# Performance work log

Hardware: AMD Instinct MI355X
Metric: run time of the kernel (lower is better)

The kernel has to match this reference:

```python
import jax, jax.numpy as jnp
import numpy as np

N_LAYERS = 32
HIDDEN = 1024
INTER = 2816
BATCH = 256
INIT_SCALE = 0.02


def setup_inputs() -> dict:
    key = jax.random.key(0)
    k_h, k_g, k_u, k_d = jax.random.split(key, 4)
    down_std = INIT_SCALE / np.sqrt(2 * N_LAYERS)
    h = jax.random.normal(k_h, (BATCH, N_LAYERS, HIDDEN), dtype=jnp.float32)
    # torch Linear weight layout: (out_features, in_features); stack over experts
    Wg = jax.random.normal(k_g, (N_LAYERS, INTER, HIDDEN), dtype=jnp.float32) * INIT_SCALE
    Wu = jax.random.normal(k_u, (N_LAYERS, INTER, HIDDEN), dtype=jnp.float32) * INIT_SCALE
    Wd = jax.random.normal(k_d, (N_LAYERS, HIDDEN, INTER), dtype=jnp.float32) * down_std
    return {"h": h, "Wg": Wg, "Wu": Wu, "Wd": Wd}


def reference(h, Wg, Wu, Wd):
    # h: (B, N, D); Wg/Wu: (N, I, D); Wd: (N, D, I)
    gate = jnp.einsum("bnd,nid->bni", h, Wg)
    up = jnp.einsum("bnd,nid->bni", h, Wu)
    act = jax.nn.silu(gate) * up            # (B, N, I)
    out = jnp.einsum("bni,ndi->bnd", act, Wd)  # (B, N, D)
    return out
```

## Files before the change

### kernel.cpp

```cpp
#include <hip/hip_runtime.h>
#include <hip/hip_bf16.h>

#define BATCH   256
#define NLAYERS 32
#define HID     1024
#define INTER   2816

typedef __attribute__((ext_vector_type(8))) short bf16x8;
typedef __attribute__((ext_vector_type(4))) float f32x4;
typedef __attribute__((ext_vector_type(4))) int   i32x4;

__device__ __forceinline__ ushort f2bf(float f) {
  __hip_bfloat16 b = __float2bfloat16(f);
  return *reinterpret_cast<ushort*>(&b);
}

__device__ __forceinline__ bf16x8 cvt8(f32x4 a, f32x4 b) {
  bf16x8 o;
  o[0] = (short)f2bf(a[0]); o[1] = (short)f2bf(a[1]);
  o[2] = (short)f2bf(a[2]); o[3] = (short)f2bf(a[3]);
  o[4] = (short)f2bf(b[0]); o[5] = (short)f2bf(b[1]);
  o[6] = (short)f2bf(b[2]); o[7] = (short)f2bf(b[3]);
  return o;
}

__global__ __launch_bounds__(256) void k_pack(
    const float* __restrict__ h, ushort* __restrict__ Xp2) {
  const int pr    = blockIdx.x * 4 + (threadIdx.x >> 6);
  const int b     = pr >> 5;
  const int layer = pr & 31;
  const int lane  = threadIdx.x & 63;
  const float* src = h + (size_t)b * (NLAYERS * HID) + (size_t)layer * HID;
  ushort* dstL = Xp2 + (size_t)layer * (32 * 8192);
#pragma unroll
  for (int c = 0; c < 2; ++c) {
    int gi = lane + c * 64;
    int t  = gi >> 2, kg = gi & 3;
    f32x4 v0 = *(const f32x4*)(src + t * 32 + kg * 8);
    f32x4 v1 = *(const f32x4*)(src + t * 32 + kg * 8 + 4);
    int f = kg ^ ((b >> 1) & 3);
    *(bf16x8*)(dstL + (size_t)t * 8192 + b * 32 + f * 8) = cvt8(v0, v1);
  }
}

__global__ __launch_bounds__(512, 4) void k_gateup(
    const ushort* __restrict__ Xp2, const float* __restrict__ Wg,
    const float* __restrict__ Wu, ushort* __restrict__ act) {
  const int bid   = blockIdx.x;
  const int layer = bid / (INTER / 64);
  const int it    = bid % (INTER / 64);
  const int i0    = it * 64;
  const int tid   = threadIdx.x;
  const int lane  = tid & 63;
  const int wave  = tid >> 6;
  const int wm    = wave >> 1;
  const int wn    = wave & 1;
  const int r16   = lane & 15;
  const int g4    = lane >> 4;

  __shared__ ushort Al[2][256 * 32];
  __shared__ ushort Bl[2][128 * 32];

  f32x4 acc[4][2][2] = {};

  const int brow  = tid >> 2;
  const int bslot = tid & 3;
  const int bdst  = brow * 32 + ((bslot ^ ((brow >> 1) & 3)) << 3);
  const float* bsrc = (brow < 64 ? Wg + (size_t)(i0 + brow) * HID
                                 : Wu + (size_t)(i0 + brow - 64) * HID)
                      + (size_t)layer * INTER * HID + bslot * 8;

  const ushort* agbase = Xp2 + (size_t)layer * (32 * 8192);

#pragma unroll
  for (int c = 0; c < 2; ++c)
    __builtin_amdgcn_global_load_lds(
        (const void*)(agbase + (wave * 128 + c * 64 + lane) * 8),
        (void*)&Al[0][(wave * 128 + c * 64) * 8], 16, 0, 0);
  {
    f32x4 rb0 = *(const f32x4*)bsrc;
    f32x4 rb1 = *(const f32x4*)(bsrc + 4);
    *(bf16x8*)&Bl[0][bdst] = cvt8(rb0, rb1);
  }
  __syncthreads();

  const int NK = HID / 32;
  int cur = 0;
  for (int t = 0; t < NK; ++t) {
    const int nxt = cur ^ 1;
    f32x4 rb[2];
    if (t + 1 < NK) {
#pragma unroll
      for (int c = 0; c < 2; ++c)
        __builtin_amdgcn_global_load_lds(
            (const void*)(agbase + (size_t)(t + 1) * 8192 +
                          (wave * 128 + c * 64 + lane) * 8),
            (void*)&Al[nxt][(wave * 128 + c * 64) * 8], 16, 0, 0);
      rb[0] = *(const f32x4*)(bsrc + (t + 1) * 32);
      rb[1] = *(const f32x4*)(bsrc + (t + 1) * 32 + 4);
    }

    bf16x8 af[4];
#pragma unroll
    for (int m = 0; m < 4; ++m) {
      int row = wm * 64 + m * 16 + r16;
      af[m] = *(bf16x8*)&Al[cur][row * 32 + ((g4 ^ ((row >> 1) & 3)) << 3)];
    }
#pragma unroll
    for (int n = 0; n < 2; ++n) {
      int rg_ = wn * 32 + n * 16 + r16;
      int ru_ = 64 + rg_;
      bf16x8 bg = *(bf16x8*)&Bl[cur][rg_ * 32 + ((g4 ^ ((rg_ >> 1) & 3)) << 3)];
      bf16x8 bu = *(bf16x8*)&Bl[cur][ru_ * 32 + ((g4 ^ ((ru_ >> 1) & 3)) << 3)];
#pragma unroll
      for (int m = 0; m < 4; ++m) {
        acc[m][n][0] = __builtin_amdgcn_mfma_f32_16x16x32_bf16(af[m], bg, acc[m][n][0], 0, 0, 0);
        acc[m][n][1] = __builtin_amdgcn_mfma_f32_16x16x32_bf16(af[m], bu, acc[m][n][1], 0, 0, 0);
      }
    }

    if (t + 1 < NK)
      *(bf16x8*)&Bl[nxt][bdst] = cvt8(rb[0], rb[1]);
    __syncthreads();
    cur = nxt;
  }

  const int r4 = (lane >> 4) * 4;
#pragma unroll
  for (int m = 0; m < 4; ++m)
#pragma unroll
    for (int n = 0; n < 2; ++n)
#pragma unroll
      for (int r = 0; r < 4; ++r) {
        float g = acc[m][n][0][r];
        float u = acc[m][n][1][r];
        float a = (g / (1.f + __expf(-g))) * u;
        int b = wm * 64 + m * 16 + r4 + r;
        int i = i0 + wn * 32 + n * 16 + r16;
        act[((size_t)layer * BATCH + b) * INTER + i] = f2bf(a);
      }
}

#define BK 64

__global__ __launch_bounds__(512) void k_down(
    const ushort* __restrict__ act, const float* __restrict__ Wd,
    float* __restrict__ out) {
  const int bid   = blockIdx.x;
  const int layer = bid / (HID / 64);
  const int dtile = bid % (HID / 64);
  const int d0    = dtile * 64;
  const int tid   = threadIdx.x;
  const int lane  = tid & 63;
  const int wave  = tid >> 6;
  const int wm    = wave >> 1;
  const int wn    = wave & 1;

  __shared__ ushort lds[BATCH * BK + 64 * BK];
  ushort* Al = lds;
  ushort* Wl = lds + BATCH * BK;

  f32x4 acc[4][2] = {};

  int aldst[4];
  const ushort* asrc[4];
#pragma unroll
  for (int r = 0; r < 4; ++r) {
    int g = tid + 512 * r;
    int arow = g >> 3, akc = g & 7;
    aldst[r] = arow * BK + ((akc ^ (arow & 7)) << 3);
    asrc[r] = act + ((size_t)layer * BATCH + arow) * INTER + akc * 8;
  }
  const int wrow = tid >> 3, wkc = tid & 7;
  const int wldst = wrow * BK + ((wkc ^ (wrow & 7)) << 3);
  const float* wsrc = Wd + (size_t)layer * HID * INTER + (size_t)(d0 + wrow) * INTER + wkc * 8;

  i32x4 ra[4];
  f32x4 rw[2];

#pragma unroll
  for (int r = 0; r < 4; ++r) ra[r] = *(const i32x4*)asrc[r];
  rw[0] = *(const f32x4*)wsrc; rw[1] = *(const f32x4*)(wsrc + 4);

  const int NK = INTER / BK;
  for (int k = 0; k < NK; ++k) {
    __syncthreads();
#pragma unroll
    for (int r = 0; r < 4; ++r) *(i32x4*)&Al[aldst[r]] = ra[r];
    *(bf16x8*)&Wl[wldst] = cvt8(rw[0], rw[1]);
    __syncthreads();

    if (k + 1 < NK) {
      int off = (k + 1) * BK;
#pragma unroll
      for (int r = 0; r < 4; ++r) ra[r] = *(const i32x4*)(asrc[r] + off);
      rw[0] = *(const f32x4*)(wsrc + off); rw[1] = *(const f32x4*)(wsrc + off + 4);
    }

#pragma unroll
    for (int ks = 0; ks < 2; ++ks) {
      const int kg = ks * 4 + (lane >> 4);
      bf16x8 af[4];
#pragma unroll
      for (int m = 0; m < 4; ++m) {
        int row = wm * 64 + m * 16 + (lane & 15);
        af[m] = *(bf16x8*)&Al[row * BK + ((kg ^ (row & 7)) << 3)];
      }
#pragma unroll
      for (int n = 0; n < 2; ++n) {
        int row = wn * 32 + n * 16 + (lane & 15);
        bf16x8 bw = *(bf16x8*)&Wl[row * BK + ((kg ^ (row & 7)) << 3)];
#pragma unroll
        for (int m = 0; m < 4; ++m)
          acc[m][n] = __builtin_amdgcn_mfma_f32_16x16x32_bf16(af[m], bw, acc[m][n], 0, 0, 0);
      }
    }
  }

  const int c16 = lane & 15;
  const int r4  = (lane >> 4) * 4;
#pragma unroll
  for (int m = 0; m < 4; ++m)
#pragma unroll
    for (int n = 0; n < 2; ++n)
#pragma unroll
      for (int r = 0; r < 4; ++r) {
        int b = wm * 64 + m * 16 + r4 + r;
        int d = d0 + wn * 32 + n * 16 + c16;
        out[(size_t)b * (NLAYERS * HID) + (size_t)layer * HID + d] = acc[m][n][r];
      }
}

extern "C" void kernel_launch(void* const* d_in, const int* in_sizes, int n_in,
                              void* d_out, int out_size, void* d_ws, size_t ws_size,
                              hipStream_t stream) {
  const float* h  = (const float*)d_in[0];
  const float* Wg = (const float*)d_in[1];
  const float* Wu = (const float*)d_in[2];
  const float* Wd = (const float*)d_in[3];
  float* out  = (float*)d_out;
  ushort* act = (ushort*)d_ws;
  ushort* Xp2 = (ushort*)d_ws + (size_t)NLAYERS * BATCH * INTER;

  hipLaunchKernelGGL(k_pack, dim3(BATCH * NLAYERS / 4), dim3(256), 0, stream,
                     h, Xp2);
  hipLaunchKernelGGL(k_gateup, dim3(NLAYERS * (INTER / 64)), dim3(512), 0, stream,
                     Xp2, Wg, Wu, act);
  hipLaunchKernelGGL(k_down, dim3(NLAYERS * (HID / 64)), dim3(512), 0, stream,
                     act, Wd, out);
}
```

Baseline: 324.8 us.

## Stream fp32 gate/up weights to LDS asynchronously with triple buffering and smaller tiles

The gate/up kernel now loads fp32 weight tiles directly into LDS with global_load_lds into a three-stage ring buffer. Conversion to bf16 happens after the LDS read instead of before the LDS write, and explicit vmcnt waits with raw barriers replace __syncthreads. The intermediate tile is halved to 32 columns, which doubles the block count, and block IDs are swizzled so that grouped blocks share a layer. The goal is to hide weight-load latency and remove register staging, at the cost of re-reading the activation tile from LDS for each smaller N-tile and doing fewer MFMAs per barrier.

New measurement: 355.8 us. 9.5% more time.

```diff
diff --git a/kernel.cpp b/kernel.cpp
--- a/kernel.cpp
+++ b/kernel.cpp
@@ -47,9 +47,10 @@
     const ushort* __restrict__ Xp2, const float* __restrict__ Wg,
     const float* __restrict__ Wu, ushort* __restrict__ act) {
   const int bid   = blockIdx.x;
-  const int layer = bid / (INTER / 64);
-  const int it    = bid % (INTER / 64);
-  const int i0    = it * 64;
+  const int swz   = (bid & 7) * 352 + (bid >> 3);
+  const int layer = swz / (INTER / 32);
+  const int it    = swz % (INTER / 32);
+  const int i0    = it * 32;
   const int tid   = threadIdx.x;
   const int lane  = tid & 63;
   const int wave  = tid >> 6;
@@ -59,86 +60,86 @@
   const int g4    = lane >> 4;
 
   __shared__ ushort Al[2][256 * 32];
-  __shared__ ushort Bl[2][128 * 32];
-
-  f32x4 acc[4][2][2] = {};
-
-  const int brow  = tid >> 2;
-  const int bslot = tid & 3;
-  const int bdst  = brow * 32 + ((bslot ^ ((brow >> 1) & 3)) << 3);
-  const float* bsrc = (brow < 64 ? Wg + (size_t)(i0 + brow) * HID
-                                 : Wu + (size_t)(i0 + brow - 64) * HID)
-                      + (size_t)layer * INTER * HID + bslot * 8;
-
-  const ushort* agbase = Xp2 + (size_t)layer * (32 * 8192);
+  __shared__ float  Bl[3][64 * 32];
+
+  f32x4 acc[4][2] = {};
+
+  const ushort* achunk = Xp2 + (size_t)layer * (32 * 8192);
+  const int arow0 = wave * 32;
+
+  const int brow = wave * 8 + (lane >> 3);
+  const int bkg  = (lane & 7) ^ ((lane >> 3) & 7);
+  const float* bptr = (brow < 32 ? Wg + (size_t)(i0 + brow) * HID
+                                 : Wu + (size_t)(i0 + brow - 32) * HID)
+                      + (size_t)layer * INTER * HID + bkg * 4;
 
 #pragma unroll
   for (int c = 0; c < 2; ++c)
     __builtin_amdgcn_global_load_lds(
-        (const void*)(agbase + (wave * 128 + c * 64 + lane) * 8),
-        (void*)&Al[0][(wave * 128 + c * 64) * 8], 16, 0, 0);
-  {
-    f32x4 rb0 = *(const f32x4*)bsrc;
-    f32x4 rb1 = *(const f32x4*)(bsrc + 4);
-    *(bf16x8*)&Bl[0][bdst] = cvt8(rb0, rb1);
-  }
-  __syncthreads();
+        (const void*)(achunk + (arow0 + c * 16) * 32 + lane * 8),
+        (void*)&Al[0][(arow0 + c * 16) * 32], 16, 0, 0);
+  __builtin_amdgcn_global_load_lds((const void*)bptr,
+                                   (void*)&Bl[0][wave * 256], 16, 0, 0);
+  __builtin_amdgcn_global_load_lds((const void*)(bptr + 32),
+                                   (void*)&Bl[1][wave * 256], 16, 0, 0);
 
   const int NK = HID / 32;
-  int cur = 0;
   for (int t = 0; t < NK; ++t) {
-    const int nxt = cur ^ 1;
-    f32x4 rb[2];
+    __builtin_amdgcn_s_barrier();
     if (t + 1 < NK) {
 #pragma unroll
       for (int c = 0; c < 2; ++c)
         __builtin_amdgcn_global_load_lds(
-            (const void*)(agbase + (size_t)(t + 1) * 8192 +
-                          (wave * 128 + c * 64 + lane) * 8),
-            (void*)&Al[nxt][(wave * 128 + c * 64) * 8], 16, 0, 0);
-      rb[0] = *(const f32x4*)(bsrc + (t + 1) * 32);
-      rb[1] = *(const f32x4*)(bsrc + (t + 1) * 32 + 4);
-    }
+            (const void*)(achunk + (size_t)(t + 1) * 8192 + (arow0 + c * 16) * 32 + lane * 8),
+            (void*)&Al[(t + 1) & 1][(arow0 + c * 16) * 32], 16, 0, 0);
+    }
+    if (t + 2 < NK)
+      __builtin_amdgcn_global_load_lds(
+          (const void*)(bptr + (t + 2) * 32),
+          (void*)&Bl[(t + 2) % 3][wave * 256], 16, 0, 0);
+
+    if (t + 2 < NK)      asm volatile("s_waitcnt vmcnt(4)" ::: "memory");
+    else if (t + 1 < NK) asm volatile("s_waitcnt vmcnt(3)" ::: "memory");
+    else                 asm volatile("s_waitcnt vmcnt(0)" ::: "memory");
+    __builtin_amdgcn_s_barrier();
+    __builtin_amdgcn_sched_barrier(0);
+
+    const ushort* As = Al[t & 1];
+    const float*  Bs = Bl[t % 3];
 
     bf16x8 af[4];
 #pragma unroll
     for (int m = 0; m < 4; ++m) {
       int row = wm * 64 + m * 16 + r16;
-      af[m] = *(bf16x8*)&Al[cur][row * 32 + ((g4 ^ ((row >> 1) & 3)) << 3)];
-    }
-#pragma unroll
-    for (int n = 0; n < 2; ++n) {
-      int rg_ = wn * 32 + n * 16 + r16;
-      int ru_ = 64 + rg_;
-      bf16x8 bg = *(bf16x8*)&Bl[cur][rg_ * 32 + ((g4 ^ ((rg_ >> 1) & 3)) << 3)];
-      bf16x8 bu = *(bf16x8*)&Bl[cur][ru_ * 32 + ((g4 ^ ((ru_ >> 1) & 3)) << 3)];
-#pragma unroll
-      for (int m = 0; m < 4; ++m) {
-        acc[m][n][0] = __builtin_amdgcn_mfma_f32_16x16x32_bf16(af[m], bg, acc[m][n][0], 0, 0, 0);
-        acc[m][n][1] = __builtin_amdgcn_mfma_f32_16x16x32_bf16(af[m], bu, acc[m][n][1], 0, 0, 0);
-      }
-    }
-
-    if (t + 1 < NK)
-      *(bf16x8*)&Bl[nxt][bdst] = cvt8(rb[0], rb[1]);
-    __syncthreads();
-    cur = nxt;
+      af[m] = *(bf16x8*)&As[row * 32 + ((g4 ^ ((row >> 1) & 3)) << 3)];
+    }
+    const int rg = wn * 16 + r16;
+    const int ru = 32 + rg;
+    f32x4 g0 = *(const f32x4*)&Bs[rg * 32 + (((2 * g4)     ^ (rg & 7)) << 2)];
+    f32x4 g1 = *(const f32x4*)&Bs[rg * 32 + (((2 * g4 + 1) ^ (rg & 7)) << 2)];
+    f32x4 u0 = *(const f32x4*)&Bs[ru * 32 + (((2 * g4)     ^ (ru & 7)) << 2)];
+    f32x4 u1 = *(const f32x4*)&Bs[ru * 32 + (((2 * g4 + 1) ^ (ru & 7)) << 2)];
+    bf16x8 bg = cvt8(g0, g1);
+    bf16x8 bu = cvt8(u0, u1);
+#pragma unroll
+    for (int m = 0; m < 4; ++m) {
+      acc[m][0] = __builtin_amdgcn_mfma_f32_16x16x32_bf16(af[m], bg, acc[m][0], 0, 0, 0);
+      acc[m][1] = __builtin_amdgcn_mfma_f32_16x16x32_bf16(af[m], bu, acc[m][1], 0, 0, 0);
+    }
   }
 
   const int r4 = (lane >> 4) * 4;
 #pragma unroll
   for (int m = 0; m < 4; ++m)
 #pragma unroll
-    for (int n = 0; n < 2; ++n)
-#pragma unroll
-      for (int r = 0; r < 4; ++r) {
-        float g = acc[m][n][0][r];
-        float u = acc[m][n][1][r];
-        float a = (g / (1.f + __expf(-g))) * u;
-        int b = wm * 64 + m * 16 + r4 + r;
-        int i = i0 + wn * 32 + n * 16 + r16;
-        act[((size_t)layer * BATCH + b) * INTER + i] = f2bf(a);
-      }
+    for (int r = 0; r < 4; ++r) {
+      float g = acc[m][0][r];
+      float u = acc[m][1][r];
+      float a = (g / (1.f + __expf(-g))) * u;
+      int b = wm * 64 + m * 16 + r4 + r;
+      int i = i0 + wn * 16 + r16;
+      act[((size_t)layer * BATCH + b) * INTER + i] = f2bf(a);
+    }
 }
 
 #define BK 64
@@ -244,7 +245,7 @@
 
   hipLaunchKernelGGL(k_pack, dim3(BATCH * NLAYERS / 4), dim3(256), 0, stream,
                      h, Xp2);
-  hipLaunchKernelGGL(k_gateup, dim3(NLAYERS * (INTER / 64)), dim3(512), 0, stream,
+  hipLaunchKernelGGL(k_gateup, dim3(NLAYERS * (INTER / 32)), dim3(512), 0, stream,
                      Xp2, Wg, Wu, act);
   hipLaunchKernelGGL(k_down, dim3(NLAYERS * (HID / 64)), dim3(512), 0, stream,
                      act, Wd, out);
```
